# Kernel optimization log

Hardware: AMD Instinct MI355X
Metric: run time of the kernel (lower is better)

The kernel has to match this reference:

```python
import jax, jax.numpy as jnp
import numpy as np

N, V, E_PER = 8, 4608, 73728          # batch, nodes per graph, edges per graph
D_IN, C, NCLS = 1, 512, 3             # node feat dim, embed dim, classes
E = N * E_PER
LN_EPS = 1e-5


def setup_inputs() -> dict:
    key = jax.random.key(0)
    ks = jax.random.split(key, 12)
    x = jax.random.normal(ks[0], (N, 1, V, D_IN), jnp.float32)
    edge_index = jax.random.randint(ks[1], (2, E), 0, V, dtype=jnp.int32)
    edge_weight = jax.random.uniform(ks[2], (E,), jnp.float32)
    # GCNConv params: layer0 maps D_IN->C, layers 1..2 map C->C (weight [in,out], bias [out])
    w0 = jax.random.normal(ks[3], (D_IN, C), jnp.float32) * 0.02
    b0 = jnp.zeros((C,), jnp.float32)
    w1 = jax.random.normal(ks[4], (C, C), jnp.float32) * 0.02
    b1 = jnp.zeros((C,), jnp.float32)
    w2 = jax.random.normal(ks[5], (C, C), jnp.float32) * 0.02
    b2 = jnp.zeros((C,), jnp.float32)
    ln_g = jnp.ones((C,), jnp.float32)
    ln_b = jnp.zeros((C,), jnp.float32)
    head_w = jax.random.normal(ks[6], (C, NCLS), jnp.float32) * 2e-5
    head_b = jnp.log(jnp.full((NCLS,), 1.0 / NCLS, jnp.float32))
    return {"x": x, "edge_weight": edge_weight, "w0": w0, "b0": b0,
            "w1": w1, "b1": b1, "w2": w2, "b2": b2,
            "ln_g": ln_g, "ln_b": ln_b, "head_w": head_w, "head_b": head_b,
            "edge_index": edge_index}


def layer_norm(h, g, b):
    mu = h.mean(-1, keepdims=True)
    var = ((h - mu) ** 2).mean(-1, keepdims=True)
    return (h - mu) * jax.lax.rsqrt(var + LN_EPS) * g + b


def reference(x, edge_weight, w0, b0, w1, b1, w2, b2, ln_g, ln_b, head_w, head_b, edge_index):
    n, t, v, d = x.shape
    nv = n * v
    h = x.reshape(nv, d)
    # batch-offset local edge indices (edges are contiguous per graph)
    offs = jnp.repeat(jnp.arange(n, dtype=edge_index.dtype) * v, edge_index.shape[1] // n)
    src = edge_index[0] + offs
    tgt = edge_index[1] + offs
    # GCN norm with self-loops (fill weight 1.0), symmetric deg^-1/2 normalization
    loop = jnp.arange(nv, dtype=src.dtype)
    src_f = jnp.concatenate([src, loop])
    tgt_f = jnp.concatenate([tgt, loop])
    ew_f = jnp.concatenate([edge_weight, jnp.ones((nv,), edge_weight.dtype)])
    deg = jax.ops.segment_sum(ew_f, tgt_f, num_segments=nv)
    deg_safe = jnp.where(deg > 0, deg, 1.0)
    dinv = jnp.where(deg > 0, jax.lax.rsqrt(deg_safe), 0.0)
    norm = dinv[src_f] * ew_f * dinv[tgt_f]
    for w, bb in ((w0, b0), (w1, b1), (w2, b2)):
        hw = h @ w                                   # [NV, C]
        msg = norm[:, None] * hw[src_f]              # gather + scale  [E+NV, C]
        h = jax.ops.segment_sum(msg, tgt_f, num_segments=nv) + bb
        h = jax.nn.relu(h)
        h = layer_norm(h, ln_g, ln_b)
        # dropout is identity in eval mode
    pooled = h.reshape(n, v, -1).max(axis=1)         # global_max_pool (contiguous batch)
    pooled = layer_norm(pooled, ln_g, ln_b)
    return pooled @ head_w + head_b                  # [N, NCLS]
```

## Files before the change

### kernel.cpp

```cpp
#include <hip/hip_runtime.h>
#include <hip/hip_bf16.h>
#include <stdint.h>

#define N_GRAPH 8
#define V_NODES 4608
#define E_PER   73728
#define NV      (N_GRAPH * V_NODES)
#define E_TOT   (N_GRAPH * E_PER)
#define C       512
#define NCLS    3
#define LN_EPS  1e-5f
#define POOL_CHUNKS 36
#define POOL_PARTS  144
#define SCAN_BLOCKS 144
#define SUBB    32
#define EPSB    (E_PER / SUBB)

typedef __attribute__((ext_vector_type(8))) short short8;
typedef __attribute__((ext_vector_type(4))) float floatx4;
typedef __attribute__((ext_vector_type(2))) float float2v;
typedef __attribute__((address_space(1))) void v_g;
typedef __attribute__((address_space(3))) void v_l;


__device__ inline float waveReduceSum(float v) {
#pragma unroll
    for (int o = 32; o > 0; o >>= 1) v += __shfl_down(v, o, 64);
    return v;
}

__device__ inline float waveAllSum(float v) {
#pragma unroll
    for (int o = 32; o > 0; o >>= 1) v += __shfl_xor(v, o, 64);
    return v;
}

__device__ inline float blockSum512(float v, volatile float* sred) {
    float s = waveReduceSum(v);
    if ((threadIdx.x & 63) == 0) sred[threadIdx.x >> 6] = s;
    __syncthreads();
    float t = 0.f;
#pragma unroll
    for (int i = 0; i < 8; i++) t += sred[i];
    __syncthreads();
    return t;
}

__device__ inline unsigned short f2bf(float f) {
    uint32_t u = __float_as_uint(f);
    u += 0x7fffu + ((u >> 16) & 1u);
    return (unsigned short)(u >> 16);
}
__device__ inline float bf2f(unsigned short b) {
    return __uint_as_float(((uint32_t)b) << 16);
}


#if __has_builtin(__builtin_amdgcn_cvt_pk_fp8_f32)
__device__ inline uint32_t pk_fp8(float a, float b) {
    return (uint32_t)__builtin_amdgcn_cvt_pk_fp8_f32(a, b, 0, false);
}
#else
__device__ inline uint32_t fp8_enc1(float f) {
    float a = fminf(fmaxf(f, -448.f), 448.f);
    uint32_t u = __float_as_uint(a);
    uint32_t s = (u >> 24) & 0x80;
    int e = (int)((u >> 23) & 0xff) - 127;
    uint32_t m = u & 0x7fffff;
    if (a == 0.f || e < -9) return s;
    if (e < -6) {
        int sh = -6 - e;
        uint32_t full = 0x800000u | m;
        uint32_t q = full >> (20 + sh);
        uint32_t rem = full & ((1u << (20 + sh)) - 1);
        uint32_t half = 1u << (19 + sh);
        q += (rem > half || (rem == half && (q & 1)));
        return s | q;
    }
    uint32_t q = m >> 20;
    uint32_t rem = m & 0xfffff;
    q += (rem > 0x80000 || (rem == 0x80000 && (q & 1)));
    uint32_t v = ((uint32_t)(e + 7) << 3) + q;
    if (v > 0x7e) v = 0x7e;
    return s | v;
}
__device__ inline uint32_t pk_fp8(float a, float b) {
    return fp8_enc1(a) | (fp8_enc1(b) << 8);
}
#endif

#if __has_builtin(__builtin_amdgcn_cvt_pk_f32_fp8)
__device__ inline float2v up_fp8_lo(uint32_t w) { return __builtin_amdgcn_cvt_pk_f32_fp8((int)w, false); }
__device__ inline float2v up_fp8_hi(uint32_t w) { return __builtin_amdgcn_cvt_pk_f32_fp8((int)w, true); }
#else
__device__ inline float fp8_dec1(uint32_t b) {
    uint32_t s = (b >> 7) & 1u, e = (b >> 3) & 0xfu, m = b & 7u;
    float mag = e ? ldexpf(1.0f + (float)m * 0.125f, (int)e - 7)
                  : (float)m * 0.001953125f;
    return s ? -mag : mag;
}
__device__ inline float2v up_fp8_lo(uint32_t w) {
    float2v r; r.x = fp8_dec1(w & 0xff); r.y = fp8_dec1((w >> 8) & 0xff); return r;
}
__device__ inline float2v up_fp8_hi(uint32_t w) {
    float2v r; r.x = fp8_dec1((w >> 16) & 0xff); r.y = fp8_dec1(w >> 24); return r;
}
#endif


__launch_bounds__(256)
__global__ void k_hist(const int* __restrict__ ei, const float* __restrict__ ew,
                       int* __restrict__ hist_c, float* __restrict__ hist_d) {
    __shared__ int   lcnt[V_NODES];
    __shared__ float ldeg[V_NODES];
    const int g = blockIdx.x >> 5, j = blockIdx.x & 31;
    const int tid = threadIdx.x;
    for (int i = tid; i < V_NODES; i += 256) { lcnt[i] = 0; ldeg[i] = 0.f; }
    __syncthreads();
    const int ebase = g * E_PER + j * EPSB;
    const int*   tgt = ei + E_TOT + ebase;
    const float* w   = ew + ebase;
    for (int i = tid; i < EPSB; i += 256) {
        int t = tgt[i];
        atomicAdd(&lcnt[t], 1);
        atomicAdd(&ldeg[t], w[i]);
    }
    __syncthreads();
    const size_t hb = ((size_t)g * SUBB + j) * V_NODES;
    for (int i = tid; i < V_NODES; i += 256) {
        hist_c[hb + i] = lcnt[i];
        hist_d[hb + i] = ldeg[i];
    }
}

__global__ void k_reduce(int* __restrict__ hist_c, const float* __restrict__ hist_d,
                         int* __restrict__ counts, float* __restrict__ dinv) {
    const int node = blockIdx.x * 256 + threadIdx.x;
    if (node >= NV) return;
    const int g = node / V_NODES, t = node - g * V_NODES;
    const size_t base = (size_t)g * SUBB * V_NODES + t;
    int c = 0;
    float d = 1.0f;
#pragma unroll 8
    for (int j = 0; j < SUBB; j++) {
        const size_t idx = base + (size_t)j * V_NODES;
        int cc = hist_c[idx];
        hist_c[idx] = c;
        c += cc;
        d += hist_d[idx];
    }
    counts[node] = c;
    dinv[node] = rsqrtf(d);
}


__global__ void k_scan1(const int* __restrict__ counts, int* __restrict__ row_ptr,
                        int* __restrict__ bsum) {
    __shared__ int sh[256];
    const int b = blockIdx.x, tid = threadIdx.x;
    const int idx = b * 256 + tid;
    int v = counts[idx];
    sh[tid] = v;
    __syncthreads();
#pragma unroll
    for (int off = 1; off < 256; off <<= 1) {
        int t = (tid >= off) ? sh[tid - off] : 0;
        __syncthreads();
        sh[tid] += t;
        __syncthreads();
    }
    row_ptr[idx] = sh[tid] - v;
    if (tid == 255) bsum[b] = sh[255];
}

__global__ void k_scan2(int* __restrict__ bsum) {
    __shared__ int sh[256];
    const int tid = threadIdx.x;
    int v = (tid < SCAN_BLOCKS) ? bsum[tid] : 0;
    sh[tid] = v;
    __syncthreads();
#pragma unroll
    for (int off = 1; off < 256; off <<= 1) {
        int t = (tid >= off) ? sh[tid - off] : 0;
        __syncthreads();
        sh[tid] += t;
        __syncthreads();
    }
    if (tid < SCAN_BLOCKS) bsum[tid] = sh[tid] - v;
}

__global__ void k_scan3(int* __restrict__ row_ptr, const int* __restrict__ bsum) {
    const int b = blockIdx.x, tid = threadIdx.x;
    const int idx = b * 256 + tid;
    row_ptr[idx] += bsum[b];
    if (idx == 0) row_ptr[NV] = E_TOT;
}

__launch_bounds__(256)
__global__ void k_fill2(const int* __restrict__ ei, const float* __restrict__ ew,
                        const float* __restrict__ dinv, const int* __restrict__ row_ptr,
                        const int* __restrict__ hist_c,
                        int* __restrict__ col_idx, float* __restrict__ val) {
    __shared__ int cur[V_NODES];
    const int g = blockIdx.x >> 5, j = blockIdx.x & 31;
    const int tid = threadIdx.x;
    const int gV = g * V_NODES;
    const size_t hb = ((size_t)g * SUBB + j) * V_NODES;
    for (int i = tid; i < V_NODES; i += 256)
        cur[i] = row_ptr[gV + i] + hist_c[hb + i];
    __syncthreads();
    const int ebase = g * E_PER + j * EPSB;
    const int*   src = ei + ebase;
    const int*   tgt = ei + E_TOT + ebase;
    const float* w   = ew + ebase;
    for (int i = tid; i < EPSB; i += 256) {
        int t = tgt[i];
        int s = src[i] + gV;
        int pos = atomicAdd(&cur[t], 1);
        col_idx[pos] = s;
        val[pos] = dinv[s] * w[i] * dinv[gV + t];
    }
}


__global__ void k_wt(const float* __restrict__ w1, const float* __restrict__ w2,
                     unsigned short* __restrict__ wt1, unsigned short* __restrict__ wt2) {
    int idx = blockIdx.x * 256 + threadIdx.x;
    int which = idx >> 18;
    int rem = idx & 0x3ffff;
    int n = rem >> 9, k = rem & 511;
    const float* W = which ? w2 : w1;
    unsigned short* WT = which ? wt2 : wt1;
    WT[n * C + k] = f2bf(W[k * C + n]);
}


__global__ void k_agg0_scalar(const float* __restrict__ x, const int* __restrict__ row_ptr,
                              const int* __restrict__ col_idx, const float* __restrict__ val,
                              const float* __restrict__ dinv, float* __restrict__ s0) {
    int t = blockIdx.x * 256 + threadIdx.x;
    if (t >= NV) return;
    float dt = dinv[t];
    float acc = dt * dt * x[t];
    int e1 = row_ptr[t + 1];
    for (int e = row_ptr[t]; e < e1; e++)
        acc += val[e] * x[col_idx[e]];
    s0[t] = acc;
}

__launch_bounds__(128)
__global__ void k_l0post(const float* __restrict__ s0, const float* __restrict__ w0,
                         const float* __restrict__ b0, const float* __restrict__ ln_g,
                         const float* __restrict__ ln_b, unsigned short* __restrict__ out) {
    const int t = blockIdx.x;
    const int tid = threadIdx.x;
    const int c4 = tid << 2;
    float s = s0[t];
    float4 w = *reinterpret_cast<const float4*>(&w0[c4]);
    float4 bb = *reinterpret_cast<const float4*>(&b0[c4]);
    float vx = fmaxf(s * w.x + bb.x, 0.f);
    float vy = fmaxf(s * w.y + bb.y, 0.f);
    float vz = fmaxf(s * w.z + bb.z, 0.f);
    float vw = fmaxf(s * w.w + bb.w, 0.f);
    __shared__ float redA[2], redB[2];
    float wsum = waveReduceSum(vx + vy + vz + vw);
    if ((tid & 63) == 0) redA[tid >> 6] = wsum;
    __syncthreads();
    float mu = (redA[0] + redA[1]) * (1.0f / C);
    float dx = vx - mu, dy = vy - mu, dz = vz - mu, dw = vw - mu;
    float wsq = waveReduceSum(dx * dx + dy * dy + dz * dz + dw * dw);
    if ((tid & 63) == 0) redB[tid >> 6] = wsq;
    __syncthreads();
    float rstd = rsqrtf((redB[0] + redB[1]) * (1.0f / C) + LN_EPS);
    float4 g = *reinterpret_cast<const float4*>(&ln_g[c4]);
    float4 b = *reinterpret_cast<const float4*>(&ln_b[c4]);
    ushort4 o = { f2bf(dx * rstd * g.x + b.x), f2bf(dy * rstd * g.y + b.y),
                  f2bf(dz * rstd * g.z + b.z), f2bf(dw * rstd * g.w + b.w) };
    reinterpret_cast<ushort4*>(out)[(size_t)t * 128 + tid] = o;
}


__launch_bounds__(256)
__global__ void k_gemm_mfma(const unsigned short* __restrict__ A,
                            const unsigned short* __restrict__ WT,
                            uint8_t* __restrict__ Bout) {
    __shared__ short8 lA[512];
    __shared__ short8 lB[512];
    const int tid = threadIdx.x;
    const int lane = tid & 63;
    const int wave = tid >> 6;
    const int wr = wave >> 1, wc = wave & 1;
    const int l15 = lane & 15, kg = lane >> 4;
    const int m0 = blockIdx.x * 128;
    const int n0 = blockIdx.y * 128;

    floatx4 acc[4][4] = {};

    const int s0i = tid, s1i = 256 + tid;
    const int kgs0 = s0i >> 7, idx0 = s0i & 127;
    const int kgs1 = s1i >> 7, idx1 = s1i & 127;
    const unsigned short* gA0 = A + (size_t)(m0 + idx0) * C + kgs0 * 8;
    const unsigned short* gA1 = A + (size_t)(m0 + idx1) * C + kgs1 * 8;
    const unsigned short* gB0 = WT + (size_t)(n0 + idx0) * C + kgs0 * 8;
    const unsigned short* gB1 = WT + (size_t)(n0 + idx1) * C + kgs1 * 8;

    for (int k0 = 0; k0 < C; k0 += 32) {
        __builtin_amdgcn_global_load_lds((v_g*)(gA0 + k0), (v_l*)&lA[s0i], 16, 0, 0);
        __builtin_amdgcn_global_load_lds((v_g*)(gA1 + k0), (v_l*)&lA[s1i], 16, 0, 0);
        __builtin_amdgcn_global_load_lds((v_g*)(gB0 + k0), (v_l*)&lB[s0i], 16, 0, 0);
        __builtin_amdgcn_global_load_lds((v_g*)(gB1 + k0), (v_l*)&lB[s1i], 16, 0, 0);
        asm volatile("s_waitcnt vmcnt(0)" ::: "memory");
        __syncthreads();

        short8 af[4], bf[4];
#pragma unroll
        for (int mi = 0; mi < 4; mi++)
            af[mi] = lA[kg * 128 + wr * 64 + mi * 16 + l15];
#pragma unroll
        for (int ni = 0; ni < 4; ni++)
            bf[ni] = lB[kg * 128 + wc * 64 + ni * 16 + l15];
#pragma unroll
        for (int mi = 0; mi < 4; mi++)
#pragma unroll
            for (int ni = 0; ni < 4; ni++)
                acc[mi][ni] = __builtin_amdgcn_mfma_f32_16x16x32_bf16(
                    af[mi], bf[ni], acc[mi][ni], 0, 0, 0);
        __syncthreads();
    }

#pragma unroll
    for (int mi = 0; mi < 4; mi++) {
#pragma unroll
        for (int ni = 0; ni < 4; ni++) {
            int n = n0 + wc * 64 + ni * 16 + l15;
            floatx4 v = acc[mi][ni];
            uint32_t p01 = pk_fp8(v[0], v[1]);
            uint32_t p23 = pk_fp8(v[2], v[3]);
            uint8_t* rp = Bout + (size_t)(m0 + wr * 64 + mi * 16 + kg * 4) * C + n;
            rp[0]     = (uint8_t)p01;
            rp[C]     = (uint8_t)(p01 >> 8);
            rp[2 * C] = (uint8_t)p23;
            rp[3 * C] = (uint8_t)(p23 >> 8);
        }
    }
}


__launch_bounds__(256)
__global__ void k_agg(const uint8_t* __restrict__ hw, const int* __restrict__ row_ptr,
                      const int* __restrict__ col_idx, const float* __restrict__ val,
                      const float* __restrict__ dinv, const float* __restrict__ bias,
                      const float* __restrict__ ln_g, const float* __restrict__ ln_b,
                      unsigned short* __restrict__ out) {
    const int b = blockIdx.x;
    const int wv = threadIdx.x >> 6;
    const int lane = threadIdx.x & 63;
    const int t = (b & 7) * V_NODES + ((b >> 3) << 2) + wv;
    const int e0 = row_ptr[t], e1 = row_ptr[t + 1];
    const uint2* hw8 = reinterpret_cast<const uint2*>(hw);

    const float dt = dinv[t];
    const float selfw = dt * dt;
    float a[8];
    {
        uint2 hv = hw8[(size_t)t * 64 + lane];
        float2v f01 = up_fp8_lo(hv.x), f23 = up_fp8_hi(hv.x);
        float2v f45 = up_fp8_lo(hv.y), f67 = up_fp8_hi(hv.y);
        a[0] = selfw * f01.x; a[1] = selfw * f01.y;
        a[2] = selfw * f23.x; a[3] = selfw * f23.y;
        a[4] = selfw * f45.x; a[5] = selfw * f45.y;
        a[6] = selfw * f67.x; a[7] = selfw * f67.y;
    }

    int e = e0;
    for (; e + 4 <= e1; e += 4) {
        int i0 = col_idx[e], i1 = col_idx[e + 1], i2 = col_idx[e + 2], i3 = col_idx[e + 3];
        float w0 = val[e], w1 = val[e + 1], w2 = val[e + 2], w3 = val[e + 3];
        uint2 h0 = hw8[(size_t)i0 * 64 + lane];
        uint2 h1 = hw8[(size_t)i1 * 64 + lane];
        uint2 h2 = hw8[(size_t)i2 * 64 + lane];
        uint2 h3 = hw8[(size_t)i3 * 64 + lane];
#define ACC8(hv, w) { \
        float2v q01 = up_fp8_lo(hv.x), q23 = up_fp8_hi(hv.x); \
        float2v q45 = up_fp8_lo(hv.y), q67 = up_fp8_hi(hv.y); \
        a[0] += (w) * q01.x; a[1] += (w) * q01.y; \
        a[2] += (w) * q23.x; a[3] += (w) * q23.y; \
        a[4] += (w) * q45.x; a[5] += (w) * q45.y; \
        a[6] += (w) * q67.x; a[7] += (w) * q67.y; }
        ACC8(h0, w0) ACC8(h1, w1) ACC8(h2, w2) ACC8(h3, w3)
    }
    for (; e < e1; e++) {
        int is = col_idx[e];
        float w = val[e];
        uint2 hv = hw8[(size_t)is * 64 + lane];
        ACC8(hv, w)
    }
#undef ACC8

    const int c8 = lane << 3;
    float4 bb0 = *reinterpret_cast<const float4*>(&bias[c8]);
    float4 bb1 = *reinterpret_cast<const float4*>(&bias[c8 + 4]);
    a[0] = fmaxf(a[0] + bb0.x, 0.f); a[1] = fmaxf(a[1] + bb0.y, 0.f);
    a[2] = fmaxf(a[2] + bb0.z, 0.f); a[3] = fmaxf(a[3] + bb0.w, 0.f);
    a[4] = fmaxf(a[4] + bb1.x, 0.f); a[5] = fmaxf(a[5] + bb1.y, 0.f);
    a[6] = fmaxf(a[6] + bb1.z, 0.f); a[7] = fmaxf(a[7] + bb1.w, 0.f);

    float s = a[0] + a[1] + a[2] + a[3] + a[4] + a[5] + a[6] + a[7];
    float mu = waveAllSum(s) * (1.0f / C);
    float sq = 0.f;
#pragma unroll
    for (int i = 0; i < 8; i++) { float d = a[i] - mu; sq += d * d; }
    float rstd = rsqrtf(waveAllSum(sq) * (1.0f / C) + LN_EPS);

    float4 g0 = *reinterpret_cast<const float4*>(&ln_g[c8]);
    float4 g1 = *reinterpret_cast<const float4*>(&ln_g[c8 + 4]);
    float4 z0 = *reinterpret_cast<const float4*>(&ln_b[c8]);
    float4 z1 = *reinterpret_cast<const float4*>(&ln_b[c8 + 4]);
    short8 o;
    o[0] = (short)f2bf((a[0] - mu) * rstd * g0.x + z0.x);
    o[1] = (short)f2bf((a[1] - mu) * rstd * g0.y + z0.y);
    o[2] = (short)f2bf((a[2] - mu) * rstd * g0.z + z0.z);
    o[3] = (short)f2bf((a[3] - mu) * rstd * g0.w + z0.w);
    o[4] = (short)f2bf((a[4] - mu) * rstd * g1.x + z1.x);
    o[5] = (short)f2bf((a[5] - mu) * rstd * g1.y + z1.y);
    o[6] = (short)f2bf((a[6] - mu) * rstd * g1.z + z1.z);
    o[7] = (short)f2bf((a[7] - mu) * rstd * g1.w + z1.w);
    reinterpret_cast<short8*>(out)[(size_t)t * 64 + lane] = o;
}


__launch_bounds__(256)
__global__ void k_pool1(const unsigned short* __restrict__ h, float* __restrict__ pmax) {
    const int g = blockIdx.x, chunk = blockIdx.y;
    const int wv = threadIdx.x >> 6, lane = threadIdx.x & 63;
    const short8* h8 = reinterpret_cast<const short8*>(h);
    const size_t r0 = (size_t)g * V_NODES + chunk * 128 + wv * 32;
    float m[8];
#pragma unroll
    for (int i = 0; i < 8; i++) m[i] = -1e30f;
    for (int r = 0; r < 32; r++) {
        short8 v = h8[(r0 + r) * 64 + lane];
#pragma unroll
        for (int i = 0; i < 8; i++) m[i] = fmaxf(m[i], bf2f((unsigned short)v[i]));
    }
    float* dst = pmax + ((size_t)(g * POOL_PARTS + chunk * 4 + wv)) * C + (lane << 3);
    float4 o0 = { m[0], m[1], m[2], m[3] };
    float4 o1 = { m[4], m[5], m[6], m[7] };
    *reinterpret_cast<float4*>(dst) = o0;
    *reinterpret_cast<float4*>(dst + 4) = o1;
}

__global__ void k_pool2_head(const float* __restrict__ pmax, const float* __restrict__ ln_g,
                             const float* __restrict__ ln_b, const float* __restrict__ hw,
                             const float* __restrict__ hb, float* __restrict__ out) {
    __shared__ float sred[8];
    int g = blockIdx.x;
    int c = threadIdx.x;
    float m = -1e30f;
    for (int j = 0; j < POOL_PARTS; j++)
        m = fmaxf(m, pmax[((size_t)g * POOL_PARTS + j) * C + c]);
    float total = blockSum512(m, sred);
    float mu = total * (1.0f / C);
    float d = m - mu;
    float var = blockSum512(d * d, sred) * (1.0f / C);
    float rstd = rsqrtf(var + LN_EPS);
    float p = d * rstd * ln_g[c] + ln_b[c];
    float r0 = blockSum512(p * hw[c * NCLS + 0], sred);
    float r1 = blockSum512(p * hw[c * NCLS + 1], sred);
    float r2 = blockSum512(p * hw[c * NCLS + 2], sred);
    if (threadIdx.x == 0) {
        out[g * NCLS + 0] = r0 + hb[0];
        out[g * NCLS + 1] = r1 + hb[1];
        out[g * NCLS + 2] = r2 + hb[2];
    }
}


extern "C" void kernel_launch(void* const* d_in, const int* in_sizes, int n_in,
                              void* d_out, int out_size, void* d_ws, size_t ws_size,
                              hipStream_t stream) {
    const float* x      = (const float*)d_in[0];
    const float* ew     = (const float*)d_in[1];
    const float* w0     = (const float*)d_in[2];
    const float* b0     = (const float*)d_in[3];
    const float* w1     = (const float*)d_in[4];
    const float* b1     = (const float*)d_in[5];
    const float* w2     = (const float*)d_in[6];
    const float* b2     = (const float*)d_in[7];
    const float* ln_g   = (const float*)d_in[8];
    const float* ln_b   = (const float*)d_in[9];
    const float* head_w = (const float*)d_in[10];
    const float* head_b = (const float*)d_in[11];
    const int*   ei     = (const int*)d_in[12];
    float* out = (float*)d_out;

    char* p = (char*)d_ws;
    auto alloc = [&](size_t bytes) { void* r = p; p += (bytes + 255) & ~255ull; return r; };
    unsigned short* bufA = (unsigned short*)alloc((size_t)NV * C * 2);
    uint8_t*        bufF = (uint8_t*)alloc((size_t)NV * C);
    unsigned short* wt1  = (unsigned short*)alloc((size_t)C * C * 2);
    unsigned short* wt2  = (unsigned short*)alloc((size_t)C * C * 2);
    float* s0      = (float*)alloc((size_t)NV * 4);
    float* dinv    = (float*)alloc((size_t)NV * 4);
    int*   counts  = (int*)alloc((size_t)NV * 4);
    int*   row_ptr = (int*)alloc((size_t)(NV + 1) * 4);
    int*   bsum    = (int*)alloc((size_t)SCAN_BLOCKS * 4);
    int*   hist_c  = (int*)alloc((size_t)N_GRAPH * SUBB * V_NODES * 4);
    float* hist_d  = (float*)alloc((size_t)N_GRAPH * SUBB * V_NODES * 4);
    int*   col_idx = (int*)alloc((size_t)E_TOT * 4);
    float* val     = (float*)alloc((size_t)E_TOT * 4);
    float* pmax    = (float*)alloc((size_t)N_GRAPH * POOL_PARTS * C * 4);

    k_hist<<<N_GRAPH * SUBB, 256, 0, stream>>>(ei, ew, hist_c, hist_d);
    k_reduce<<<SCAN_BLOCKS, 256, 0, stream>>>(hist_c, hist_d, counts, dinv);
    k_scan1<<<SCAN_BLOCKS, 256, 0, stream>>>(counts, row_ptr, bsum);
    k_scan2<<<1, 256, 0, stream>>>(bsum);
    k_scan3<<<SCAN_BLOCKS, 256, 0, stream>>>(row_ptr, bsum);
    k_fill2<<<N_GRAPH * SUBB, 256, 0, stream>>>(ei, ew, dinv, row_ptr, hist_c, col_idx, val);
    k_wt<<<(2 * C * C) / 256, 256, 0, stream>>>(w1, w2, wt1, wt2);

    k_agg0_scalar<<<NV / 256, 256, 0, stream>>>(x, row_ptr, col_idx, val, dinv, s0);
    k_l0post<<<NV, 128, 0, stream>>>(s0, w0, b0, ln_g, ln_b, bufA);

    k_gemm_mfma<<<dim3(NV / 128, C / 128), 256, 0, stream>>>(bufA, wt1, bufF);
    k_agg<<<NV / 4, 256, 0, stream>>>(bufF, row_ptr, col_idx, val, dinv, b1, ln_g, ln_b, bufA);

    k_gemm_mfma<<<dim3(NV / 128, C / 128), 256, 0, stream>>>(bufA, wt2, bufF);
    k_agg<<<NV / 4, 256, 0, stream>>>(bufF, row_ptr, col_idx, val, dinv, b2, ln_g, ln_b, bufA);

    k_pool1<<<dim3(N_GRAPH, POOL_CHUNKS), 256, 0, stream>>>(bufA, pmax);
    k_pool2_head<<<N_GRAPH, C, 0, stream>>>(pmax, ln_g, ln_b, head_w, head_b, out);
}
```

Measured before the change: 369.4 us.

## Fuse layer-0 scalar aggregation into CSR fill via shared-memory partial sums

The layer-0 scalar aggregation kernel is removed. The CSR fill kernel now also accumulates val*x[src] per target node into shared-memory partial sums, one per sub-block, and writes them into the reused hist_d buffer. k_l0post then reduces the 32 partials per node and adds the self-loop term. This drops one kernel launch and its gather pass over the CSR, at the cost of shared-memory float atomics in the fill kernel and a nondeterministic summation order.

```diff
diff --git a/kernel.cpp b/kernel.cpp
--- a/kernel.cpp
+++ b/kernel.cpp
@@ -199,15 +199,19 @@
 __launch_bounds__(256)
 __global__ void k_fill2(const int* __restrict__ ei, const float* __restrict__ ew,
                         const float* __restrict__ dinv, const int* __restrict__ row_ptr,
-                        const int* __restrict__ hist_c,
-                        int* __restrict__ col_idx, float* __restrict__ val) {
-    __shared__ int cur[V_NODES];
+                        const int* __restrict__ hist_c, const float* __restrict__ x,
+                        int* __restrict__ col_idx, float* __restrict__ val,
+                        float* __restrict__ hist_s) {
+    __shared__ int   cur[V_NODES];
+    __shared__ float sacc[V_NODES];
     const int g = blockIdx.x >> 5, j = blockIdx.x & 31;
     const int tid = threadIdx.x;
     const int gV = g * V_NODES;
     const size_t hb = ((size_t)g * SUBB + j) * V_NODES;
-    for (int i = tid; i < V_NODES; i += 256)
+    for (int i = tid; i < V_NODES; i += 256) {
         cur[i] = row_ptr[gV + i] + hist_c[hb + i];
+        sacc[i] = 0.f;
+    }
     __syncthreads();
     const int ebase = g * E_PER + j * EPSB;
     const int*   src = ei + ebase;
@@ -216,10 +220,15 @@
     for (int i = tid; i < EPSB; i += 256) {
         int t = tgt[i];
         int s = src[i] + gV;
+        float v = dinv[s] * w[i] * dinv[gV + t];
         int pos = atomicAdd(&cur[t], 1);
         col_idx[pos] = s;
-        val[pos] = dinv[s] * w[i] * dinv[gV + t];
-    }
+        val[pos] = v;
+        atomicAdd(&sacc[t], v * x[s]);
+    }
+    __syncthreads();
+    for (int i = tid; i < V_NODES; i += 256)
+        hist_s[hb + i] = sacc[i];
 }
 
 
@@ -235,27 +244,28 @@
 }
 
 
-__global__ void k_agg0_scalar(const float* __restrict__ x, const int* __restrict__ row_ptr,
-                              const int* __restrict__ col_idx, const float* __restrict__ val,
-                              const float* __restrict__ dinv, float* __restrict__ s0) {
-    int t = blockIdx.x * 256 + threadIdx.x;
-    if (t >= NV) return;
-    float dt = dinv[t];
-    float acc = dt * dt * x[t];
-    int e1 = row_ptr[t + 1];
-    for (int e = row_ptr[t]; e < e1; e++)
-        acc += val[e] * x[col_idx[e]];
-    s0[t] = acc;
-}
-
 __launch_bounds__(128)
-__global__ void k_l0post(const float* __restrict__ s0, const float* __restrict__ w0,
-                         const float* __restrict__ b0, const float* __restrict__ ln_g,
-                         const float* __restrict__ ln_b, unsigned short* __restrict__ out) {
-    const int t = blockIdx.x;
+__global__ void k_l0post(const float* __restrict__ x, const float* __restrict__ dinv,
+                         const float* __restrict__ hist_s,
+                         const float* __restrict__ w0, const float* __restrict__ b0,
+                         const float* __restrict__ ln_g, const float* __restrict__ ln_b,
+                         unsigned short* __restrict__ out) {
+    const int node = blockIdx.x;
     const int tid = threadIdx.x;
+    const int g = node / V_NODES, t = node - g * V_NODES;
+    __shared__ float s_sh;
+    if (tid < 32) {
+        float p = hist_s[((size_t)g * SUBB + tid) * V_NODES + t];
+#pragma unroll
+        for (int o = 16; o > 0; o >>= 1) p += __shfl_xor(p, o, 32);
+        if (tid == 0) {
+            float dt = dinv[node];
+            s_sh = dt * dt * x[node] + p;
+        }
+    }
+    __syncthreads();
+    const float s = s_sh;
     const int c4 = tid << 2;
-    float s = s0[t];
     float4 w = *reinterpret_cast<const float4*>(&w0[c4]);
     float4 bb = *reinterpret_cast<const float4*>(&b0[c4]);
     float vx = fmaxf(s * w.x + bb.x, 0.f);
@@ -272,11 +282,11 @@
     if ((tid & 63) == 0) redB[tid >> 6] = wsq;
     __syncthreads();
     float rstd = rsqrtf((redB[0] + redB[1]) * (1.0f / C) + LN_EPS);
-    float4 g = *reinterpret_cast<const float4*>(&ln_g[c4]);
+    float4 gg = *reinterpret_cast<const float4*>(&ln_g[c4]);
     float4 b = *reinterpret_cast<const float4*>(&ln_b[c4]);
-    ushort4 o = { f2bf(dx * rstd * g.x + b.x), f2bf(dy * rstd * g.y + b.y),
-                  f2bf(dz * rstd * g.z + b.z), f2bf(dw * rstd * g.w + b.w) };
-    reinterpret_cast<ushort4*>(out)[(size_t)t * 128 + tid] = o;
+    ushort4 o = { f2bf(dx * rstd * gg.x + b.x), f2bf(dy * rstd * gg.y + b.y),
+                  f2bf(dz * rstd * gg.z + b.z), f2bf(dw * rstd * gg.w + b.w) };
+    reinterpret_cast<ushort4*>(out)[(size_t)node * 128 + tid] = o;
 }
 
 
@@ -500,7 +510,6 @@
     uint8_t*        bufF = (uint8_t*)alloc((size_t)NV * C);
     unsigned short* wt1  = (unsigned short*)alloc((size_t)C * C * 2);
     unsigned short* wt2  = (unsigned short*)alloc((size_t)C * C * 2);
-    float* s0      = (float*)alloc((size_t)NV * 4);
     float* dinv    = (float*)alloc((size_t)NV * 4);
     int*   counts  = (int*)alloc((size_t)NV * 4);
     int*   row_ptr = (int*)alloc((size_t)(NV + 1) * 4);
@@ -516,11 +525,11 @@
     k_scan1<<<SCAN_BLOCKS, 256, 0, stream>>>(counts, row_ptr, bsum);
     k_scan2<<<1, 256, 0, stream>>>(bsum);
     k_scan3<<<SCAN_BLOCKS, 256, 0, stream>>>(row_ptr, bsum);
-    k_fill2<<<N_GRAPH * SUBB, 256, 0, stream>>>(ei, ew, dinv, row_ptr, hist_c, col_idx, val);
+    k_fill2<<<N_GRAPH * SUBB, 256, 0, stream>>>(ei, ew, dinv, row_ptr, hist_c, x,
+                                                col_idx, val, hist_d);
     k_wt<<<(2 * C * C) / 256, 256, 0, stream>>>(w1, w2, wt1, wt2);
 
-    k_agg0_scalar<<<NV / 256, 256, 0, stream>>>(x, row_ptr, col_idx, val, dinv, s0);
-    k_l0post<<<NV, 128, 0, stream>>>(s0, w0, b0, ln_g, ln_b, bufA);
+    k_l0post<<<NV, 128, 0, stream>>>(x, dinv, hist_d, w0, b0, ln_g, ln_b, bufA);
 
     k_gemm_mfma<<<dim3(NV / 128, C / 128), 256, 0, stream>>>(bufA, wt1, bufF);
     k_agg<<<NV / 4, 256, 0, stream>>>(bufF, row_ptr, col_idx, val, dinv, b1, ln_g, ln_b, bufA);
```

Measured after the change: 368.8 us. No clear change (-0.2%).
